# Performance work log

Hardware: AMD Instinct MI355X
Metric: run time of the kernel (lower is better)

The kernel has to match this reference:

```python
import jax, jax.numpy as jnp
import numpy as np

NUM_HEADS = 16
BLOCK_KV = 64


def _split_heads(x, h):
    B, T, D = x.shape
    return x.reshape(B, T, h, D // h).transpose(0, 2, 1, 3)  # [B,H,T,Hd]


def _merge_heads(x):
    B, H, T, Hd = x.shape
    return x.transpose(0, 2, 1, 3).reshape(B, T, H * Hd)


def _streaming_attention(qh, kh, vh, bkv):
    # Online-softmax (flash-attention) over kv blocks; math identical to the
    # original nested-loop version (including the Z + 1e-9 denominator).
    B, H, T, Dh = qh.shape
    scale = 1.0 / jnp.sqrt(Dh).astype(jnp.float32)
    q32 = qh.astype(jnp.float32)
    nb = T // bkv
    # [nb, B, H, bkv, Dh]
    kb = jnp.moveaxis(kh.astype(jnp.float32).reshape(B, H, nb, bkv, Dh), 2, 0)
    vb = jnp.moveaxis(vh.astype(jnp.float32).reshape(B, H, nb, bkv, Dh), 2, 0)

    def step(carry, blk):
        m, Z, O = carry
        k_blk, v_blk = blk
        scores = jnp.einsum('bhtd,bhkd->bhtk', q32, k_blk) * scale
        m_new = jnp.maximum(m, jnp.max(scores, axis=-1, keepdims=True))
        alpha = jnp.exp(m - m_new)
        p = jnp.exp(scores - m_new)
        Z = Z * alpha + jnp.sum(p, axis=-1, keepdims=True)
        O = O * alpha + jnp.einsum('bhtk,bhkd->bhtd', p, v_blk)
        return (m_new, Z, O), None

    m0 = jnp.full((B, H, T, 1), -jnp.inf, dtype=jnp.float32)
    Z0 = jnp.zeros((B, H, T, 1), dtype=jnp.float32)
    O0 = jnp.zeros((B, H, T, Dh), dtype=jnp.float32)
    (m, Z, O), _ = jax.lax.scan(step, (m0, Z0, O0), (kb, vb))
    return (O / (Z + 1e-9)).astype(qh.dtype)


def setup_inputs() -> dict:
    key = jax.random.key(0)
    ks = jax.random.split(key, 6)
    B, T, D = 4, 8192, 512
    s = 1.0 / np.sqrt(D)
    return {
        'x': jax.random.normal(ks[0], (B, T, D), dtype=jnp.float32),
        'Wq': jax.random.normal(ks[1], (D, D), dtype=jnp.float32) * s,
        'Wk': jax.random.normal(ks[2], (D, D), dtype=jnp.float32) * s,
        'Wv': jax.random.normal(ks[3], (D, D), dtype=jnp.float32) * s,
        'Wo': jax.random.normal(ks[4], (D, D), dtype=jnp.float32) * s,
        'bo': jnp.zeros((D,), dtype=jnp.float32),
    }


def reference(x, Wq, Wk, Wv, Wo, bo):
    q = x @ Wq
    k = x @ Wk
    v = x @ Wv
    qh = _split_heads(q, NUM_HEADS)
    kh = _split_heads(k, NUM_HEADS)
    vh = _split_heads(v, NUM_HEADS)
    out_h = _streaming_attention(qh, kh, vh, BLOCK_KV)
    return _merge_heads(out_h) @ Wo + bo
```

## Files before the change

kernel.cpp:

```cpp
#include <hip/hip_runtime.h>
#include <hip/hip_bf16.h>
#include <math.h>

typedef __bf16 bf16;
typedef __bf16 bf16x2 __attribute__((ext_vector_type(2)));
typedef __bf16 bf16x4 __attribute__((ext_vector_type(4)));
typedef __bf16 bf16x8 __attribute__((ext_vector_type(8)));
typedef float f32x4 __attribute__((ext_vector_type(4)));
typedef unsigned int u32;
typedef u32 u32x4 __attribute__((ext_vector_type(4)));

#define B_ 4
#define T_ 8192
#define D_ 512
#define H_ 16
#define HD_ 32
#define M_ (B_ * T_)

#if __has_builtin(__builtin_amdgcn_exp2f)
#define EXP2(x) __builtin_amdgcn_exp2f(x)
#else
#define EXP2(x) exp2f(x)
#endif

static __device__ __forceinline__ u32 pkbf16(float a, float b) {
  bf16x2 t;
  t[0] = (bf16)a;
  t[1] = (bf16)b;
  return __builtin_bit_cast(u32, t);
}

static __device__ __forceinline__ void swap32(u32& a, u32& b) {
#if __has_builtin(__builtin_amdgcn_permlane32_swap)
  auto r = __builtin_amdgcn_permlane32_swap(a, b, false, false);
  a = r[0];
  b = r[1];
#else
  asm volatile("v_permlane32_swap_b32 %0, %1" : "+v"(a), "+v"(b));
#endif
}

__global__ void k_cvt(const float* __restrict__ in, bf16* __restrict__ out, int n4) {
  int i = blockIdx.x * blockDim.x + threadIdx.x;
  const int stride = gridDim.x * blockDim.x;
  for (; i < n4; i += stride) {
    const float4 v = ((const float4*)in)[i];
    bf16x4 o;
    o.x = (bf16)v.x; o.y = (bf16)v.y; o.z = (bf16)v.z; o.w = (bf16)v.w;
    ((bf16x4*)out)[i] = o;
  }
}

__global__ void k_cvt_T(const float* __restrict__ w, bf16* __restrict__ wT, float scale) {
  const int tid = blockIdx.x * blockDim.x + threadIdx.x;
  const int n = tid >> 9, k = tid & 511;
  wT[tid] = (bf16)(w[k * 512 + n] * scale);
}

__global__ __launch_bounds__(256) void k_transposeV(const bf16* __restrict__ V,
                                                    bf16* __restrict__ VT) {
  __shared__ bf16 tile[128][36];
  const int bh = blockIdx.y, chunk = blockIdx.x;
  const int b = bh >> 4, h = bh & 15;
  const int kv0 = chunk * 128;
  const int tid = threadIdx.x;
  const int r = tid >> 1, c0 = (tid & 1) * 16;
  const size_t ib = ((size_t)(b * T_ + kv0 + r)) * 512 + h * 32 + c0;
  *(bf16x8*)&tile[r][c0]     = *(const bf16x8*)&V[ib];
  *(bf16x8*)&tile[r][c0 + 8] = *(const bf16x8*)&V[ib + 8];
  __syncthreads();
  const int d = tid >> 3, j0 = (tid & 7) * 16;
  bf16x8 o0, o1;
#pragma unroll
  for (int i = 0; i < 4; ++i) {
    o0[i]     = tile[j0 + i][d];
    o0[i + 4] = tile[j0 + 8 + i][d];
    o1[i]     = tile[j0 + 4 + i][d];
    o1[i + 4] = tile[j0 + 12 + i][d];
  }
  const size_t ob = ((size_t)bh * 32 + d) * T_ + kv0 + j0;
  *(bf16x8*)&VT[ob] = o0;
  *(bf16x8*)&VT[ob + 8] = o1;
}

template <int OUTF32>
__global__ __launch_bounds__(256) void k_gemm(const bf16* __restrict__ A,
                                              const bf16* __restrict__ BT,
                                              void* __restrict__ Cout,
                                              const float* __restrict__ bias) {
  __shared__ bf16 As[128][40];
  __shared__ bf16 Bs[128][40];
  const int bn = blockIdx.x * 128;
  const int bm = blockIdx.y * 128;
  const int tid = threadIdx.x;
  const int l = tid & 63, wid = tid >> 6;
  const int ln = l & 15, ku = l >> 4;
  const int wm = (wid >> 1) * 64, wn = (wid & 1) * 64;
  const int sr = tid >> 2, sc = (tid & 3) * 8;

  f32x4 acc[4][4] = {};

  for (int ks = 0; ks < 512; ks += 32) {
    __syncthreads();
    *(bf16x8*)&As[sr][sc]      = *(const bf16x8*)&A[(size_t)(bm + sr) * 512 + ks + sc];
    *(bf16x8*)&As[sr + 64][sc] = *(const bf16x8*)&A[(size_t)(bm + sr + 64) * 512 + ks + sc];
    *(bf16x8*)&Bs[sr][sc]      = *(const bf16x8*)&BT[(size_t)(bn + sr) * 512 + ks + sc];
    *(bf16x8*)&Bs[sr + 64][sc] = *(const bf16x8*)&BT[(size_t)(bn + sr + 64) * 512 + ks + sc];
    __syncthreads();

    bf16x8 af[4], bfr[4];
#pragma unroll
    for (int mt = 0; mt < 4; ++mt) af[mt] = *(const bf16x8*)&As[wm + mt * 16 + ln][ku * 8];
#pragma unroll
    for (int nt = 0; nt < 4; ++nt) bfr[nt] = *(const bf16x8*)&Bs[wn + nt * 16 + ln][ku * 8];
#pragma unroll
    for (int mt = 0; mt < 4; ++mt)
#pragma unroll
      for (int nt = 0; nt < 4; ++nt)
        acc[mt][nt] = __builtin_amdgcn_mfma_f32_16x16x32_bf16(af[mt], bfr[nt], acc[mt][nt], 0, 0, 0);
  }

#pragma unroll
  for (int mt = 0; mt < 4; ++mt)
#pragma unroll
    for (int nt = 0; nt < 4; ++nt)
#pragma unroll
      for (int r = 0; r < 4; ++r) {
        const int row = bm + wm + mt * 16 + ku * 4 + r;
        const int col = bn + wn + nt * 16 + ln;
        const float v = acc[mt][nt][r];
        if (OUTF32)
          ((float*)Cout)[(size_t)row * 512 + col] = v + bias[col];
        else
          ((bf16*)Cout)[(size_t)row * 512 + col] = (bf16)v;
      }
}

__global__ __launch_bounds__(256, 3) void k_attn(const bf16* __restrict__ Q,
                                                 const bf16* __restrict__ K,
                                                 const bf16* __restrict__ VT,
                                                 bf16* __restrict__ O) {
  __shared__ bf16 ks[2][64][40];
  __shared__ bf16 vts[2][32][72];
  const int qt = blockIdx.x;
  const int bh = blockIdx.y;
  const int b = bh >> 4, h = bh & 15;
  const size_t base = (size_t)b * T_ * 512 + (size_t)h * 32;
  const size_t vtbase = (size_t)bh * 32 * T_;
  const int tid = threadIdx.x;
  const int l = tid & 63, w = tid >> 6;
  const int ln = l & 15, ku = l >> 4;

  const int q0 = qt * 128 + w * 32;
  bf16x8 qf[2];
#pragma unroll
  for (int j = 0; j < 2; ++j)
    qf[j] = *(const bf16x8*)&Q[base + (size_t)(q0 + j * 16 + ln) * 512 + ku * 8];

  const int krow = tid >> 2, kch = (tid & 3) * 8;
  const int vrow = tid >> 3, vch = (tid & 7) * 8;

  float z[2] = {0.f, 0.f};
  f32x4 o[2][2] = {};

  {
    const bf16x8 kin = *(const bf16x8*)&K[base + (size_t)krow * 512 + kch];
    const bf16x8 vin = *(const bf16x8*)&VT[vtbase + (size_t)vrow * T_ + vch];
    *(bf16x8*)&ks[0][krow][kch] = kin;
    *(bf16x8*)&vts[0][vrow][vch] = vin;
  }
  __syncthreads();

#define KV_BODY(KB, CUR, NXT)                                                          \
  {                                                                                    \
    const int nkv0 = ((KB) + 1) * 64;                                                  \
    const bf16x8 kin = *(const bf16x8*)&K[base + (size_t)(nkv0 + krow) * 512 + kch];   \
    const bf16x8 vin = *(const bf16x8*)&VT[vtbase + (size_t)vrow * T_ + nkv0 + vch];   \
    bf16x8 kf[4];                                                                      \
    _Pragma("unroll") for (int t = 0; t < 4; ++t)                                      \
        kf[t] = *(const bf16x8*)&ks[CUR][t * 16 + ln][ku * 8];                         \
    bf16x8 va[2][2];                                                                   \
    _Pragma("unroll") for (int c = 0; c < 2; ++c)                                      \
        _Pragma("unroll") for (int hh = 0; hh < 2; ++hh)                               \
            va[c][hh] = *(const bf16x8*)&vts[CUR][hh * 16 + ln][c * 32 + ku * 8];      \
    _Pragma("unroll") for (int j = 0; j < 2; ++j) {                                    \
      f32x4 s[4];                                                                      \
      const f32x4 zz = {};                                                             \
      _Pragma("unroll") for (int t = 0; t < 4; ++t)                                    \
          s[t] = __builtin_amdgcn_mfma_f32_16x16x32_bf16(kf[t], qf[j], zz, 0, 0, 0);   \
      u32 lo[4], hi[4];                                                                \
      float ps = 0.f;                                                                  \
      _Pragma("unroll") for (int t = 0; t < 4; ++t) {                                  \
        const float a0 = EXP2(s[t][0]), a1 = EXP2(s[t][1]);                            \
        const float a2 = EXP2(s[t][2]), a3 = EXP2(s[t][3]);                            \
        ps += (a0 + a1) + (a2 + a3);                                                   \
        lo[t] = pkbf16(a0, a1);                                                        \
        hi[t] = pkbf16(a2, a3);                                                        \
      }                                                                                \
      z[j] += ps;                                                                      \
      _Pragma("unroll") for (int c = 0; c < 2; ++c) {                                  \
        u32 d0 = lo[2 * c], d2 = lo[2 * c + 1];                                        \
        swap32(d0, d2);                                                                \
        u32 d1 = hi[2 * c], d3 = hi[2 * c + 1];                                        \
        swap32(d1, d3);                                                                \
        u32x4 pd = {d0, d1, d2, d3};                                                   \
        const bf16x8 pf = __builtin_bit_cast(bf16x8, pd);                              \
        o[j][0] = __builtin_amdgcn_mfma_f32_16x16x32_bf16(va[c][0], pf, o[j][0], 0, 0, 0); \
        o[j][1] = __builtin_amdgcn_mfma_f32_16x16x32_bf16(va[c][1], pf, o[j][1], 0, 0, 0); \
      }                                                                                \
    }                                                                                  \
    *(bf16x8*)&ks[NXT][krow][kch] = kin;                                               \
    *(bf16x8*)&vts[NXT][vrow][vch] = vin;                                              \
    __syncthreads();                                                                   \
  }

  for (int kb = 0; kb < 128; kb += 2) {
    KV_BODY(kb, 0, 1);
    KV_BODY(kb + 1, 1, 0);
  }
#undef KV_BODY

#pragma unroll
  for (int j = 0; j < 2; ++j) {
    float zj = z[j];
    zj += __shfl_xor(zj, 16);
    zj += __shfl_xor(zj, 32);
    const float iz = 1.0f / (zj + 1e-9f);
    bf16x4 w0, w1;
#pragma unroll
    for (int r = 0; r < 4; ++r) {
      w0[r] = (bf16)(o[j][0][r] * iz);
      w1[r] = (bf16)(o[j][1][r] * iz);
    }
    const size_t row = base + (size_t)(q0 + j * 16 + ln) * 512;
    *(bf16x4*)&O[row + ku * 4] = w0;
    *(bf16x4*)&O[row + 16 + ku * 4] = w1;
  }
}

extern "C" void kernel_launch(void* const* d_in, const int* in_sizes, int n_in,
                              void* d_out, int out_size, void* d_ws, size_t ws_size,
                              hipStream_t stream) {
  const float* x = (const float*)d_in[0];
  const float* Wq = (const float*)d_in[1];
  const float* Wk = (const float*)d_in[2];
  const float* Wv = (const float*)d_in[3];
  const float* Wo = (const float*)d_in[4];
  const float* bo = (const float*)d_in[5];
  float* out = (float*)d_out;

  char* ws = (char*)d_ws;
  const size_t SZ = (size_t)M_ * 512 * sizeof(bf16);
  bf16* xb = (bf16*)(ws);
  bf16* qb = (bf16*)(ws + SZ);
  bf16* kb = (bf16*)(ws + 2 * SZ);
  bf16* vb = (bf16*)(ws + 3 * SZ);
  bf16* ob = (bf16*)(ws + 4 * SZ);
  bf16* wqT = (bf16*)(ws + 5 * SZ);
  bf16* wkT = wqT + 512 * 512;
  bf16* wvT = wkT + 512 * 512;
  bf16* woT = wvT + 512 * 512;
  bf16* vt = xb;

  const float SCALE_L2E = 0.17677669529663687f * 1.4426950408889634f;

  k_cvt<<<2048, 256, 0, stream>>>(x, xb, M_ * 512 / 4);
  k_cvt_T<<<1024, 256, 0, stream>>>(Wq, wqT, SCALE_L2E);
  k_cvt_T<<<1024, 256, 0, stream>>>(Wk, wkT, 1.0f);
  k_cvt_T<<<1024, 256, 0, stream>>>(Wv, wvT, 1.0f);
  k_cvt_T<<<1024, 256, 0, stream>>>(Wo, woT, 1.0f);

  dim3 gg(4, 256);
  k_gemm<0><<<gg, 256, 0, stream>>>(xb, wqT, qb, nullptr);
  k_gemm<0><<<gg, 256, 0, stream>>>(xb, wkT, kb, nullptr);
  k_gemm<0><<<gg, 256, 0, stream>>>(xb, wvT, vb, nullptr);

  dim3 gt(64, 64);
  k_transposeV<<<gt, 256, 0, stream>>>(vb, vt);
  dim3 ga(64, 64);
  k_attn<<<ga, 256, 0, stream>>>(qb, kb, vt, ob);

  k_gemm<1><<<gg, 256, 0, stream>>>(ob, woT, out, bo);
}
```

Baseline: 871.9 us.

## Stream K/V into swizzled LDS via direct global-to-LDS loads, row-sum via MFMA

Replaces the register-staged K/V double-buffer copy with __builtin_amdgcn_global_load_lds, which writes global data straight into LDS. The padded LDS arrays become unpadded XOR-swizzled layouts, so bank conflicts are avoided without the padding and shared memory per block shrinks. The softmax denominator is now accumulated by an extra MFMA against a ones vector, replacing the scalar sums and the final cross-lane shuffles. Occupancy hint rises from 3 to 5 blocks per CU. Correctness depends on the direct LDS loads completing before the barrier and on the swizzle matching on both the write and read sides.

```diff
diff --git a/kernel.cpp b/kernel.cpp
--- a/kernel.cpp
+++ b/kernel.cpp
@@ -22,6 +22,9 @@
 #else
 #define EXP2(x) exp2f(x)
 #endif
+
+#define LDSP(p) ((__attribute__((address_space(3))) void*)(p))
+#define GLBP(p) ((const __attribute__((address_space(1))) void*)(p))
 
 static __device__ __forceinline__ u32 pkbf16(float a, float b) {
   bf16x2 t;
@@ -136,12 +139,12 @@
       }
 }
 
-__global__ __launch_bounds__(256, 3) void k_attn(const bf16* __restrict__ Q,
+__global__ __launch_bounds__(256, 5) void k_attn(const bf16* __restrict__ Q,
                                                  const bf16* __restrict__ K,
                                                  const bf16* __restrict__ VT,
                                                  bf16* __restrict__ O) {
-  __shared__ bf16 ks[2][64][40];
-  __shared__ bf16 vts[2][32][72];
+  __shared__ bf16 ks[2][64][32];
+  __shared__ bf16 vts[2][32][64];
   const int qt = blockIdx.x;
   const int bh = blockIdx.y;
   const int b = bh >> 4, h = bh & 15;
@@ -157,75 +160,77 @@
   for (int j = 0; j < 2; ++j)
     qf[j] = *(const bf16x8*)&Q[base + (size_t)(q0 + j * 16 + ln) * 512 + ku * 8];
 
-  const int krow = tid >> 2, kch = (tid & 3) * 8;
-  const int vrow = tid >> 3, vch = (tid & 7) * 8;
-
-  float z[2] = {0.f, 0.f};
+  const u32 one2 = 0x3F803F80u;
+  u32x4 onesu = {one2, one2, one2, one2};
+  const bf16x8 ones = __builtin_bit_cast(bf16x8, onesu);
+
+  const int krow = tid >> 2;
+  const int kchS = ((tid & 3) ^ ((krow >> 1) & 3)) * 8;
+  const int vrow = tid >> 3;
+  const int vchS = ((tid & 7) ^ (vrow & 7)) * 8;
+  const bf16* gk = K + base + (size_t)krow * 512 + kchS;
+  const bf16* gv = VT + vtbase + (size_t)vrow * T_ + vchS;
+
+  bf16* dk0 = &ks[0][w * 16][0];
+  bf16* dk1 = &ks[1][w * 16][0];
+  bf16* dv0 = &vts[0][w * 8][0];
+  bf16* dv1 = &vts[1][w * 8][0];
+
+  const char* ksr = (const char*)&ks[0][0][0] + ln * 64 + 16 * (ku ^ ((ln >> 1) & 3));
+  const char* vr0 = (const char*)&vts[0][0][0] + ln * 128 + 16 * ((ku) ^ (ln & 7));
+  const char* vr1 = (const char*)&vts[0][0][0] + ln * 128 + 16 * ((4 + ku) ^ (ln & 7));
+
   f32x4 o[2][2] = {};
-
-  {
-    const bf16x8 kin = *(const bf16x8*)&K[base + (size_t)krow * 512 + kch];
-    const bf16x8 vin = *(const bf16x8*)&VT[vtbase + (size_t)vrow * T_ + vch];
-    *(bf16x8*)&ks[0][krow][kch] = kin;
-    *(bf16x8*)&vts[0][vrow][vch] = vin;
-  }
+  f32x4 zacc[2] = {};
+
+  __builtin_amdgcn_global_load_lds(GLBP(gk), LDSP(dk0), 16, 0, 0);
+  __builtin_amdgcn_global_load_lds(GLBP(gv), LDSP(dv0), 16, 0, 0);
+  gk += 64 * 512;
+  gv += 64;
   __syncthreads();
 
-#define KV_BODY(KB, CUR, NXT)                                                          \
-  {                                                                                    \
-    const int nkv0 = ((KB) + 1) * 64;                                                  \
-    const bf16x8 kin = *(const bf16x8*)&K[base + (size_t)(nkv0 + krow) * 512 + kch];   \
-    const bf16x8 vin = *(const bf16x8*)&VT[vtbase + (size_t)vrow * T_ + nkv0 + vch];   \
-    bf16x8 kf[4];                                                                      \
-    _Pragma("unroll") for (int t = 0; t < 4; ++t)                                      \
-        kf[t] = *(const bf16x8*)&ks[CUR][t * 16 + ln][ku * 8];                         \
-    bf16x8 va[2][2];                                                                   \
-    _Pragma("unroll") for (int c = 0; c < 2; ++c)                                      \
-        _Pragma("unroll") for (int hh = 0; hh < 2; ++hh)                               \
-            va[c][hh] = *(const bf16x8*)&vts[CUR][hh * 16 + ln][c * 32 + ku * 8];      \
-    _Pragma("unroll") for (int j = 0; j < 2; ++j) {                                    \
-      f32x4 s[4];                                                                      \
-      const f32x4 zz = {};                                                             \
-      _Pragma("unroll") for (int t = 0; t < 4; ++t)                                    \
-          s[t] = __builtin_amdgcn_mfma_f32_16x16x32_bf16(kf[t], qf[j], zz, 0, 0, 0);   \
-      u32 lo[4], hi[4];                                                                \
-      float ps = 0.f;                                                                  \
-      _Pragma("unroll") for (int t = 0; t < 4; ++t) {                                  \
-        const float a0 = EXP2(s[t][0]), a1 = EXP2(s[t][1]);                            \
-        const float a2 = EXP2(s[t][2]), a3 = EXP2(s[t][3]);                            \
-        ps += (a0 + a1) + (a2 + a3);                                                   \
-        lo[t] = pkbf16(a0, a1);                                                        \
-        hi[t] = pkbf16(a2, a3);                                                        \
-      }                                                                                \
-      z[j] += ps;                                                                      \
-      _Pragma("unroll") for (int c = 0; c < 2; ++c) {                                  \
-        u32 d0 = lo[2 * c], d2 = lo[2 * c + 1];                                        \
-        swap32(d0, d2);                                                                \
-        u32 d1 = hi[2 * c], d3 = hi[2 * c + 1];                                        \
-        swap32(d1, d3);                                                                \
-        u32x4 pd = {d0, d1, d2, d3};                                                   \
-        const bf16x8 pf = __builtin_bit_cast(bf16x8, pd);                              \
-        o[j][0] = __builtin_amdgcn_mfma_f32_16x16x32_bf16(va[c][0], pf, o[j][0], 0, 0, 0); \
-        o[j][1] = __builtin_amdgcn_mfma_f32_16x16x32_bf16(va[c][1], pf, o[j][1], 0, 0, 0); \
-      }                                                                                \
-    }                                                                                  \
-    *(bf16x8*)&ks[NXT][krow][kch] = kin;                                               \
-    *(bf16x8*)&vts[NXT][vrow][vch] = vin;                                              \
-    __syncthreads();                                                                   \
+#define KV_BODY(CUR, DKN, DVN)                                                        \
+  {                                                                                   \
+    __builtin_amdgcn_global_load_lds(GLBP(gk), LDSP(DKN), 16, 0, 0);                  \
+    __builtin_amdgcn_global_load_lds(GLBP(gv), LDSP(DVN), 16, 0, 0);                  \
+    gk += 64 * 512;                                                                   \
+    gv += 64;                                                                         \
+    _Pragma("unroll") for (int j = 0; j < 2; ++j) {                                   \
+      _Pragma("unroll") for (int c = 0; c < 2; ++c) {                                 \
+        const bf16x8 kf0 = *(const bf16x8*)(ksr + (CUR)*4096 + c * 2048);             \
+        const bf16x8 kf1 = *(const bf16x8*)(ksr + (CUR)*4096 + c * 2048 + 1024);      \
+        const f32x4 zz = {};                                                          \
+        f32x4 s0 = __builtin_amdgcn_mfma_f32_16x16x32_bf16(kf0, qf[j], zz, 0, 0, 0);  \
+        f32x4 s1 = __builtin_amdgcn_mfma_f32_16x16x32_bf16(kf1, qf[j], zz, 0, 0, 0);  \
+        u32 lo0 = pkbf16(EXP2(s0[0]), EXP2(s0[1]));                                   \
+        u32 hi0 = pkbf16(EXP2(s0[2]), EXP2(s0[3]));                                   \
+        u32 lo1 = pkbf16(EXP2(s1[0]), EXP2(s1[1]));                                   \
+        u32 hi1 = pkbf16(EXP2(s1[2]), EXP2(s1[3]));                                   \
+        swap32(lo0, lo1);                                                             \
+        swap32(hi0, hi1);                                                             \
+        u32x4 pd = {lo0, hi0, lo1, hi1};                                              \
+        const bf16x8 pf = __builtin_bit_cast(bf16x8, pd);                             \
+        const bf16x8 va0 =                                                            \
+            *(const bf16x8*)((c ? vr1 : vr0) + (CUR)*4096);                           \
+        const bf16x8 va1 =                                                            \
+            *(const bf16x8*)((c ? vr1 : vr0) + (CUR)*4096 + 2048);                    \
+        o[j][0] = __builtin_amdgcn_mfma_f32_16x16x32_bf16(va0, pf, o[j][0], 0, 0, 0); \
+        o[j][1] = __builtin_amdgcn_mfma_f32_16x16x32_bf16(va1, pf, o[j][1], 0, 0, 0); \
+        zacc[j] = __builtin_amdgcn_mfma_f32_16x16x32_bf16(ones, pf, zacc[j], 0, 0, 0);\
+      }                                                                               \
+    }                                                                                 \
+    __syncthreads();                                                                  \
   }
 
   for (int kb = 0; kb < 128; kb += 2) {
-    KV_BODY(kb, 0, 1);
-    KV_BODY(kb + 1, 1, 0);
+    KV_BODY(0, dk1, dv1);
+    KV_BODY(1, dk0, dv0);
   }
 #undef KV_BODY
 
 #pragma unroll
   for (int j = 0; j < 2; ++j) {
-    float zj = z[j];
-    zj += __shfl_xor(zj, 16);
-    zj += __shfl_xor(zj, 32);
-    const float iz = 1.0f / (zj + 1e-9f);
+    const float iz = 1.0f / (zacc[j][0] + 1e-9f);
     bf16x4 w0, w1;
 #pragma unroll
     for (int r = 0; r < 4; ++r) {
```

Result: faster. 832.6 us (-4.5%).
